# Kernel optimization log

Measured on AMD Instinct MI355X. Metric: run time of the kernel, lower is better.

Reference implementation:

```python
import jax, jax.numpy as jnp
import numpy as np

B, S, DIM = 4, 2048, 2048
H = 16
NOPE, ROPE, VD = 128, 64, 128
QKD = NOPE + ROPE            # 192
KVR = 512                    # kv_lora_rank
SCALE = QKD ** -0.5


def rms_norm(x, w, eps=1e-6):
    return x * jax.lax.rsqrt(jnp.mean(x * x, axis=-1, keepdims=True) + eps) * w


def rotary(x, cos, sin):
    # x: (b, s, h, r) with consecutive (real, imag) pairs; cos/sin: (s, r//2)
    xr, xi = x[..., 0::2], x[..., 1::2]
    c = cos[None, :, None, :]
    s_ = sin[None, :, None, :]
    yr = xr * c - xi * s_
    yi = xr * s_ + xi * c
    # re-interleave pairs -> (..., r)
    return jnp.stack([yr, yi], axis=-1).reshape(x.shape)


def setup_inputs() -> dict:
    key = jax.random.key(0)
    ks = jax.random.split(key, 6)
    w = 0.02
    x = jax.random.normal(ks[0], (B, S, DIM), jnp.float32)
    wq = jax.random.normal(ks[1], (DIM, H * QKD), jnp.float32) * w
    wkv_a = jax.random.normal(ks[2], (DIM, KVR + ROPE), jnp.float32) * w
    kv_norm_w = jnp.ones((KVR,), jnp.float32)
    wkv_b = jax.random.normal(ks[3], (H * (NOPE + VD), KVR), jnp.float32) * w
    wo = jax.random.normal(ks[4], (H * VD, DIM), jnp.float32) * w
    # standard RoPE frequencies for the 64-dim decoupled rope component
    inv_freq = 1.0 / (10000.0 ** (np.arange(0, ROPE, 2, dtype=np.float32) / ROPE))
    t = np.arange(S, dtype=np.float32)
    ang = np.outer(t, inv_freq)  # (S, ROPE//2)
    freqs_cos = jnp.asarray(np.cos(ang), jnp.float32)
    freqs_sin = jnp.asarray(np.sin(ang), jnp.float32)
    # causal mask (start_pos = 0 prefill)
    mask = jnp.where(jnp.triu(jnp.ones((S, S), bool), k=1), jnp.float32(-1e9), jnp.float32(0.0))
    return {"x": x, "wq": wq, "wkv_a": wkv_a, "kv_norm_w": kv_norm_w,
            "wkv_b": wkv_b, "wo": wo, "freqs_cos": freqs_cos,
            "freqs_sin": freqs_sin, "mask": mask}


def reference(x, wq, wkv_a, kv_norm_w, wkv_b, wo, freqs_cos, freqs_sin, mask):
    b, s, _ = x.shape
    # query projection and nope/rope split
    q = (x @ wq).reshape(b, s, H, QKD)
    q_nope, q_pe = q[..., :NOPE], q[..., NOPE:]
    q_pe = rotary(q_pe, freqs_cos, freqs_sin)                 # (b,s,H,ROPE)
    # kv low-rank latent + decoupled rope key
    kv_full = x @ wkv_a                                       # (b,t,KVR+ROPE)
    kv, k_pe = kv_full[..., :KVR], kv_full[..., KVR:]
    k_pe = rotary(k_pe[:, :, None, :], freqs_cos, freqs_sin)[:, :, 0, :]  # (b,t,ROPE)
    # absorb q_nope through wkv_b's key half
    w_b = wkv_b.reshape(H, NOPE + VD, KVR)
    q_abs = jnp.einsum('bshd,hdc->bshc', q_nope, w_b[:, :NOPE])  # (b,s,H,KVR)
    kv_c = rms_norm(kv, kv_norm_w)                            # latent kv cache (b,t,KVR)
    # two-term scores in latent + rope space
    scores = (jnp.einsum('bshc,btc->bsht', q_abs, kv_c)
              + jnp.einsum('bshr,btr->bsht', q_pe, k_pe)) * SCALE
    scores = scores + mask[None, :, None, :]
    attn = jax.nn.softmax(scores.astype(jnp.float32), axis=-1).astype(x.dtype)
    # attend in latent space, then expand with wkv_b's value half
    o = jnp.einsum('bsht,btc->bshc', attn, kv_c)
    o = jnp.einsum('bshc,hdc->bshd', o, w_b[:, NOPE:])        # (b,s,H,VD)
    return o.reshape(b, s, H * VD) @ wo
```

## Files before the change

kernel.cpp:

```cpp
#include <hip/hip_runtime.h>
#include <hip/hip_bf16.h>
#include <cstdio>
#include <cstdint>

#define BB   4
#define SS   2048
#define DIMM 2048
#define HH   16
#define NOPED 128
#define QKD  192
#define KVR  512
#define DQK  576
#define SCALE_F 0.07216878364870323f

typedef __attribute__((ext_vector_type(4))) float f32x4;
typedef __attribute__((ext_vector_type(8))) __bf16 bf16x8;
typedef __attribute__((ext_vector_type(8))) unsigned short u16x8;

__device__ __forceinline__ f32x4 mfma16(bf16x8 a, bf16x8 b, f32x4 c) {
  return __builtin_amdgcn_mfma_f32_16x16x32_bf16(a, b, c, 0, 0, 0);
}

__device__ __forceinline__ void gl16(const __bf16* g, __bf16* l) {
  __builtin_amdgcn_global_load_lds(
      (const __attribute__((address_space(1))) unsigned int*)g,
      (__attribute__((address_space(3))) unsigned int*)l, 16, 0, 0);
}

__global__ void k_cvt(const float* __restrict__ in, __bf16* __restrict__ out, int n) {
  int i = (blockIdx.x * 256 + threadIdx.x) * 8;
  if (i >= n) return;
  float4 a = *(const float4*)(in + i);
  float4 b = *(const float4*)(in + i + 4);
  bf16x8 v;
  v[0] = (__bf16)a.x; v[1] = (__bf16)a.y; v[2] = (__bf16)a.z; v[3] = (__bf16)a.w;
  v[4] = (__bf16)b.x; v[5] = (__bf16)b.y; v[6] = (__bf16)b.z; v[7] = (__bf16)b.w;
  *(bf16x8*)(out + i) = v;
}

__global__ void k_tr(const float* __restrict__ in, __bf16* __restrict__ out,
                     int R, int C, int64_t inBS, int64_t outBS) {
  in  += (int64_t)blockIdx.z * inBS;
  out += (int64_t)blockIdx.z * outBS;
  __shared__ float t[32][33];
  int c0 = blockIdx.x * 32, r0 = blockIdx.y * 32;
#pragma unroll
  for (int i = 0; i < 4; i++) {
    int r = r0 + threadIdx.y + i * 8, c = c0 + threadIdx.x;
    if (r < R && c < C) t[threadIdx.y + i * 8][threadIdx.x] = in[(int64_t)r * C + c];
  }
  __syncthreads();
#pragma unroll
  for (int i = 0; i < 4; i++) {
    int c = c0 + threadIdx.y + i * 8, r = r0 + threadIdx.x;
    if (c < C && r < R) out[(int64_t)c * R + r] = (__bf16)t[threadIdx.x][threadIdx.y + i * 8];
  }
}

template <bool OUTF32>
__global__ __launch_bounds__(256) void k_gemm(
    const __bf16* __restrict__ A, const __bf16* __restrict__ Bt, void* __restrict__ Cv,
    int N, int K, int lda, int ldb, int ldc,
    int64_t aSB, int64_t aSH, int64_t bSH, int64_t cSB, int64_t cSH, int Hdiv, float scale) {
  const int z = blockIdx.z;
  const int zb = z / Hdiv, zh = z % Hdiv;
  const int64_t aBase = zb * aSB + zh * aSH;
  const int64_t bBase = zh * bSH;
  const int64_t cBase = zb * cSB + zh * cSH;
  const int n0 = blockIdx.x * 128, m0 = blockIdx.y * 128;
  const int tid = threadIdx.x, lane = tid & 63, wid = tid >> 6;
  const int p = lane & 15, g = lane >> 4;
  const int wr = (wid >> 1) * 64, wc = (wid & 1) * 64;
  __shared__ alignas(16) __bf16 lA[128 * 32];
  __shared__ alignas(16) __bf16 lB[128 * 32];
  const f32x4 fz = {};
  f32x4 acc[4][4];
#pragma unroll
  for (int i = 0; i < 4; i++)
#pragma unroll
    for (int j = 0; j < 4; j++) acc[i][j] = fz;
  const __bf16* gA0 = A + aBase + (int64_t)(m0 + (tid >> 2)) * lda + (tid & 3) * 8;
  const __bf16* gA1 = A + aBase + (int64_t)(m0 + 64 + (tid >> 2)) * lda + (tid & 3) * 8;
  const __bf16* gB0 = Bt + bBase + (int64_t)(n0 + (tid >> 2)) * ldb + (tid & 3) * 8;
  const __bf16* gB1 = Bt + bBase + (int64_t)(n0 + 64 + (tid >> 2)) * ldb + (tid & 3) * 8;
  auto stage = [&](int kt) {
    gl16(gA0 + kt, &lA[tid * 8]);
    gl16(gA1 + kt, &lA[(256 + tid) * 8]);
    gl16(gB0 + kt, &lB[tid * 8]);
    gl16(gB1 + kt, &lB[(256 + tid) * 8]);
  };
  stage(0);
  for (int kt = 0; kt < K; kt += 32) {
    asm volatile("s_waitcnt vmcnt(0)" ::: "memory");
    __builtin_amdgcn_s_barrier();
    bf16x8 af[4], bfr[4];
#pragma unroll
    for (int mi = 0; mi < 4; mi++) af[mi]  = *(const bf16x8*)&lA[(wr + mi * 16 + p) * 32 + g * 8];
#pragma unroll
    for (int ni = 0; ni < 4; ni++) bfr[ni] = *(const bf16x8*)&lB[(wc + ni * 16 + p) * 32 + g * 8];
#pragma unroll
    for (int mi = 0; mi < 4; mi++)
#pragma unroll
      for (int ni = 0; ni < 4; ni++) acc[mi][ni] = mfma16(af[mi], bfr[ni], acc[mi][ni]);
    asm volatile("s_waitcnt lgkmcnt(0)" ::: "memory");
    __builtin_amdgcn_s_barrier();
    if (kt + 32 < K) stage(kt + 32);
  }
#pragma unroll
  for (int mi = 0; mi < 4; mi++) {
#pragma unroll
    for (int ni = 0; ni < 4; ni++) {
      const int n = n0 + wc + ni * 16 + p;
      if (n < N) {
#pragma unroll
        for (int r = 0; r < 4; r++) {
          const int m = m0 + wr + mi * 16 + g * 4 + r;
          float v = acc[mi][ni][r] * scale;
          if (OUTF32) ((float*)Cv)[cBase + (int64_t)m * ldc + n] = v;
          else        ((__bf16*)Cv)[cBase + (int64_t)m * ldc + n] = (__bf16)v;
        }
      }
    }
  }
}

__global__ __launch_bounds__(64) void k_kvprep(
    const __bf16* __restrict__ kvfull, const float* __restrict__ wnorm,
    const float* __restrict__ fc, const float* __restrict__ fs,
    __bf16* __restrict__ Kcat) {
  const int row = blockIdx.x;
  const int lane = threadIdx.x;
  const int s = row & 2047;
  const __bf16* src = kvfull + (int64_t)row * DQK;
  bf16x8 v = *(const bf16x8*)(src + lane * 8);
  float f[8], ss = 0.f;
#pragma unroll
  for (int j = 0; j < 8; j++) { f[j] = (float)v[j]; ss += f[j] * f[j]; }
#pragma unroll
  for (int mk = 1; mk < 64; mk <<= 1) ss += __shfl_xor(ss, mk, 64);
  float rn = rsqrtf(ss * (1.f / 512.f) + 1e-6f);
  bf16x8 o;
#pragma unroll
  for (int j = 0; j < 8; j++) o[j] = (__bf16)(f[j] * rn * wnorm[lane * 8 + j]);
  *(bf16x8*)(Kcat + (int64_t)row * DQK + lane * 8) = o;
  if (lane < 32) {
    float xr = (float)src[512 + 2 * lane];
    float xi = (float)src[512 + 2 * lane + 1];
    float c = fc[s * 32 + lane], sn = fs[s * 32 + lane];
    Kcat[(int64_t)row * DQK + 512 + 2 * lane]     = (__bf16)(xr * c - xi * sn);
    Kcat[(int64_t)row * DQK + 512 + 2 * lane + 1] = (__bf16)(xr * sn + xi * c);
  }
}

__global__ void k_qpe(const __bf16* __restrict__ qfull, const float* __restrict__ fc,
                      const float* __restrict__ fs, __bf16* __restrict__ Qcat) {
  int idx = blockIdx.x * 256 + threadIdx.x;
  if (idx >= BB * HH * SS * 32) return;
  int i = idx & 31, s = (idx >> 5) & 2047, h = (idx >> 16) & 15, b = idx >> 20;
  const __bf16* src = qfull + ((int64_t)(b * SS + s)) * 3072 + h * QKD + NOPED;
  float xr = (float)src[2 * i], xi = (float)src[2 * i + 1];
  float c = fc[s * 32 + i], sn = fs[s * 32 + i];
  __bf16* dst = Qcat + (((int64_t)(b * HH + h)) * SS + s) * DQK + 512;
  dst[2 * i]     = (__bf16)((xr * c - xi * sn) * SCALE_F);
  dst[2 * i + 1] = (__bf16)((xr * sn + xi * c) * SCALE_F);
}

__global__ __launch_bounds__(256, 2) void k_attn(
    const __bf16* __restrict__ Qcat, const __bf16* __restrict__ Kcat,
    const __bf16* __restrict__ Vt2, __bf16* __restrict__ Ohead) {
  const int gx = blockIdx.x;
  const int w  = blockIdx.y;
  const int z  = gx * 8 + (w & 7);
  const int yv = w >> 3;
  const int kk = yv >> 2, cc = yv & 3;
  const int bx = (kk & 1) ? (31 - ((kk - 1) << 1) - cc) : ((kk << 1) + cc);
  const int b = z >> 4, h = z & 15;
  const int q0 = bx * 64;
  const int tid = threadIdx.x, lane = tid & 63, wid = tid >> 6;
  const int p = lane & 15, g = lane >> 4;
  const int qw = q0 + wid * 16;
  __shared__ alignas(16) __bf16 lK[32 * 576];
  __shared__ alignas(16) __bf16 lV[128 * 32];
  __shared__ alignas(16) __bf16 lP[4 * 512];

  bf16x8 qreg[18];
  {
    const __bf16* qb = Qcat + ((int64_t)z * SS + qw + p) * DQK + g * 8;
#pragma unroll
    for (int kc = 0; kc < 18; kc++) qreg[kc] = *(const bf16x8*)(qb + kc * 32);
  }
  bf16x8 ones;
#pragma unroll
  for (int j = 0; j < 8; j++) ones[j] = (__bf16)1.0f;
  const f32x4 fz = {};
  f32x4 acc[8];
#pragma unroll
  for (int ct = 0; ct < 8; ct++) acc[ct] = fz;
  float mrun[4] = {-1e30f, -1e30f, -1e30f, -1e30f};
  float lrun[4] = {0.f, 0.f, 0.f, 0.f};

  const __bf16* kBase = Kcat + (int64_t)b * SS * DQK;
  const __bf16* vBase = Vt2 + (int64_t)z * 128 * SS;

  auto stage = [&](int t0) {
    const __bf16* kb = kBase + (int64_t)t0 * DQK;
#pragma unroll
    for (int it = 0; it < 9; it++) {
      int slot = it * 256 + tid;
      int row = slot / 72, u = slot - row * 72;
      gl16(kb + row * DQK + ((u ^ (row & 7)) * 8), &lK[(it * 256 + tid) * 8]);
    }
    const __bf16* vb = vBase + t0;
#pragma unroll
    for (int it = 0; it < 2; it++) {
      int slot = it * 256 + tid;
      int c = slot >> 2, u = slot & 3;
      gl16(vb + c * SS + ((u ^ ((c >> 1) & 3)) * 8), &lV[(it * 256 + tid) * 8]);
    }
  };

  const int nsteps = bx * 2 + 2;
  stage(0);
  const int vkey = (p >> 1) & 3;
  for (int st = 0; st < nsteps; st++) {
    const int t0 = st * 32;
    asm volatile("s_waitcnt vmcnt(0)" ::: "memory");
    __builtin_amdgcn_s_barrier();

    __builtin_amdgcn_s_setprio(1);
    f32x4 sca[2], scb[2];
    sca[0] = fz; sca[1] = fz; scb[0] = fz; scb[1] = fz;
#pragma unroll
    for (int kc = 0; kc < 18; kc += 2) {
#pragma unroll
      for (int n = 0; n < 2; n++) {
        int trow = n * 16 + p;
        bf16x8 bf0 = *(const bf16x8*)&lK[trow * 576 + (((4 * kc + g) ^ (trow & 7))) * 8];
        bf16x8 bf1 = *(const bf16x8*)&lK[trow * 576 + (((4 * (kc + 1) + g) ^ (trow & 7))) * 8];
        sca[n] = mfma16(qreg[kc], bf0, sca[n]);
        scb[n] = mfma16(qreg[kc + 1], bf1, scb[n]);
      }
    }
    __builtin_amdgcn_s_setprio(0);
    f32x4 sc[2];
#pragma unroll
    for (int n = 0; n < 2; n++)
#pragma unroll
      for (int r = 0; r < 4; r++) sc[n][r] = sca[n][r] + scb[n][r];
    if (t0 + 31 > qw) {
#pragma unroll
      for (int n = 0; n < 2; n++) {
        int t = t0 + n * 16 + p;
#pragma unroll
        for (int r = 0; r < 4; r++) {
          int q = qw + g * 4 + r;
          if (t > q) sc[n][r] = -1e9f;
        }
      }
    }

    float es[4];
    int needAny = 0;
#pragma unroll
    for (int r = 0; r < 4; r++) {
      float mx = fmaxf(sc[0][r], sc[1][r]);
#pragma unroll
      for (int mk = 1; mk < 16; mk <<= 1) mx = fmaxf(mx, __shfl_xor(mx, mk, 64));
      if (mx > mrun[r] + 8.f) { es[r] = __expf(mrun[r] - mx); mrun[r] = mx; needAny = 1; }
      else es[r] = 1.f;
      float s0 = __expf(sc[0][r] - mrun[r]);
      float s1 = __expf(sc[1][r] - mrun[r]);
      int prow = g * 4 + r;
      int swz = ((prow >> 1) & 3) * 8;
      lP[wid * 512 + prow * 32 + (p ^ swz)]        = (__bf16)s0;
      lP[wid * 512 + prow * 32 + ((16 + p) ^ swz)] = (__bf16)s1;
    }
    if (__any(needAny)) {
#pragma unroll
      for (int ct = 0; ct < 8; ct++)
#pragma unroll
        for (int r = 0; r < 4; r++) acc[ct][r] *= es[r];
    }
    bf16x8 pa = *(const bf16x8*)&lP[wid * 512 + p * 32 + ((g ^ vkey) * 8)];
    {
      f32x4 rs = mfma16(pa, ones, fz);
#pragma unroll
      for (int r = 0; r < 4; r++) lrun[r] = lrun[r] * es[r] + rs[r];
    }

    __builtin_amdgcn_s_setprio(1);
#pragma unroll
    for (int ct = 0; ct < 8; ct++) {
      int c = ct * 16 + p;
      bf16x8 bv = *(const bf16x8*)&lV[c * 32 + ((g ^ vkey) * 8)];
      acc[ct] = mfma16(pa, bv, acc[ct]);
    }
    __builtin_amdgcn_s_setprio(0);
    asm volatile("s_waitcnt lgkmcnt(0)" ::: "memory");
    __builtin_amdgcn_s_barrier();
    if (st + 1 < nsteps) stage(t0 + 32);
  }

#pragma unroll
  for (int r = 0; r < 4; r++) {
    float inv = 1.f / lrun[r];
    int64_t rb = ((int64_t)b * SS + qw + g * 4 + r) * 2048 + h * 128;
#pragma unroll
    for (int ct = 0; ct < 8; ct++) Ohead[rb + ct * 16 + p] = (__bf16)(acc[ct][r] * inv);
  }
}

extern "C" void kernel_launch(void* const* d_in, const int* in_sizes, int n_in,
                              void* d_out, int out_size, void* d_ws, size_t ws_size,
                              hipStream_t stream) {
  const float* x     = (const float*)d_in[0];
  const float* wq    = (const float*)d_in[1];
  const float* wkv_a = (const float*)d_in[2];
  const float* kvw   = (const float*)d_in[3];
  const float* wkv_b = (const float*)d_in[4];
  const float* wo    = (const float*)d_in[5];
  const float* fc    = (const float*)d_in[6];
  const float* fs    = (const float*)d_in[7];
  float* out = (float*)d_out;

  char* base = (char*)d_ws;
  const size_t OFF_KCAT  = 0;
  const size_t OFF_VT    = OFF_KCAT + 9437184ull;
  const size_t OFF_WKVB  = OFF_VT + 8388608ull;
  const size_t OFF_WOT   = OFF_WKVB + 4194304ull;
  const size_t OFF_QCAT  = OFF_WOT + 8388608ull;
  const size_t OFF_OHEAD = OFF_QCAT + 150994944ull;
  const size_t OFF_QFULL = OFF_OHEAD + 33554432ull;
  const size_t TOTAL     = OFF_QFULL + 50331648ull;

  __bf16* Kcat    = (__bf16*)(base + OFF_KCAT);
  __bf16* wkvb_bf = (__bf16*)(base + OFF_WKVB);
  __bf16* woT     = (__bf16*)(base + OFF_WOT);
  __bf16* Qcat    = (__bf16*)(base + OFF_QCAT);
  __bf16* o_head  = (__bf16*)(base + OFF_OHEAD);
  __bf16* qfull   = (__bf16*)(base + OFF_QFULL);
  __bf16* Vt2     = (__bf16*)(base + OFF_QFULL);
  __bf16* wqT    = (__bf16*)(base + OFF_KCAT);
  __bf16* wkvaT  = (__bf16*)(base + OFF_KCAT + 12582912);
  __bf16* xb     = (__bf16*)(base + OFF_QCAT);
  __bf16* kvfull = (__bf16*)(base + OFF_QCAT + 33554432);
  __bf16* wbTn   = (__bf16*)(base + OFF_OHEAD);

  if (ws_size < TOTAL) {
    fprintf(stderr, "kernel_launch: ws too small: need %zu have %zu\n", TOTAL, ws_size);
    return;
  }

  k_cvt<<<8192, 256, 0, stream>>>(x, xb, BB * SS * DIMM);
  k_cvt<<<1024, 256, 0, stream>>>(wkv_b, wkvb_bf, 4096 * 512);
  k_tr<<<dim3(96, 64, 1), dim3(32, 8), 0, stream>>>(wq, wqT, 2048, 3072, 0, 0);
  k_tr<<<dim3(18, 64, 1), dim3(32, 8), 0, stream>>>(wkv_a, wkvaT, 2048, 576, 0, 0);
  k_tr<<<dim3(64, 64, 1), dim3(32, 8), 0, stream>>>(wo, woT, 2048, 2048, 0, 0);
  k_tr<<<dim3(16, 4, 16), dim3(32, 8), 0, stream>>>(wkv_b, wbTn, 128, 512,
                                                    (int64_t)256 * 512, (int64_t)512 * 128);
  k_gemm<false><<<dim3(24, 64, 1), 256, 0, stream>>>(
      xb, wqT, qfull, 3072, 2048, 2048, 2048, 3072, 0, 0, 0, 0, 0, 1, 1.0f);
  k_gemm<false><<<dim3(5, 64, 1), 256, 0, stream>>>(
      xb, wkvaT, kvfull, 576, 2048, 2048, 2048, 576, 0, 0, 0, 0, 0, 1, 1.0f);
  k_kvprep<<<8192, 64, 0, stream>>>(kvfull, kvw, fc, fs, Kcat);
  k_gemm<false><<<dim3(4, 16, 64), 256, 0, stream>>>(
      qfull, wbTn, Qcat, 512, 128, 3072, 128, 576,
      (int64_t)SS * 3072, (int64_t)QKD, (int64_t)512 * 128,
      (int64_t)HH * SS * DQK, (int64_t)SS * DQK, 16, SCALE_F);
  k_qpe<<<16384, 256, 0, stream>>>(qfull, fc, fs, Qcat);
  k_gemm<false><<<dim3(16, 1, 64), 256, 0, stream>>>(
      wkvb_bf + 128 * 512, Kcat, Vt2, 2048, 512, 512, DQK, 2048,
      (int64_t)256 * 512, 0, (int64_t)SS * DQK,
      (int64_t)128 * 2048, (int64_t)16 * 128 * 2048, 4, 1.0f);
  k_attn<<<dim3(8, 256), 256, 0, stream>>>(Qcat, Kcat, Vt2, o_head);
  k_gemm<true><<<dim3(16, 64, 1), 256, 0, stream>>>(
      o_head, woT, out, 2048, 2048, 2048, 2048, 2048, 0, 0, 0, 0, 0, 1, 1.0f);
}
```

Baseline: 772.4 us.

## Use 256x256-tile 512-thread GEMM for Q and output projections

Adds a new GEMM kernel with 256x256 output tiles, 8 waves per block, double-buffered LDS staging through global_load_lds with XOR swizzle, and raised wave priority around the MFMA loop. The Q projection and the final output projection now use it instead of the generic 128x128-style kernel. Larger tiles raise arithmetic intensity and cut global/L2 traffic per FLOP. In exchange they use 128KB of LDS per block and a large accumulator footprint, so occupancy drops, and the grid shrinks to 384 and 256 blocks on a 256-CU part, which risks wave-quantization tail effects.

```diff
diff --git a/kernel.cpp b/kernel.cpp
--- a/kernel.cpp
+++ b/kernel.cpp
@@ -124,6 +124,85 @@
   }
 }
 
+template <bool OUTF32>
+__global__ __launch_bounds__(512) void k_gemm2(
+    const __bf16* __restrict__ A, const __bf16* __restrict__ Bt, void* __restrict__ Cv,
+    int K, int lda, int ldb, int ldc, float scale) {
+  const int n0 = blockIdx.x * 256, m0 = blockIdx.y * 256;
+  const int tid = threadIdx.x, lane = tid & 63, wid = tid >> 6;
+  const int p = lane & 15, g = lane >> 4;
+  const int wm = wid >> 2, wn = wid & 3;
+  __shared__ alignas(16) __bf16 lA[2][256 * 64];
+  __shared__ alignas(16) __bf16 lB[2][256 * 64];
+  const f32x4 fz = {};
+  f32x4 acc[8][4];
+#pragma unroll
+  for (int m = 0; m < 8; m++)
+#pragma unroll
+    for (int n = 0; n < 4; n++) acc[m][n] = fz;
+
+  const int sr = tid >> 3, sg = tid & 7;
+  const int scol = ((sg ^ (sr & 7)) * 8);
+  const __bf16* gA = A + (int64_t)(m0 + sr) * lda + scol;
+  const __bf16* gB = Bt + (int64_t)(n0 + sr) * ldb + scol;
+  auto stage = [&](int t, int buf) {
+    const __bf16* a = gA + t * 64;
+    const __bf16* b = gB + t * 64;
+#pragma unroll
+    for (int it = 0; it < 4; it++) {
+      gl16(a + (int64_t)(it * 64) * lda, &lA[buf][(it * 512 + tid) * 8]);
+      gl16(b + (int64_t)(it * 64) * ldb, &lB[buf][(it * 512 + tid) * 8]);
+    }
+  };
+
+  const int nt = K >> 6;
+  stage(0, 0);
+  for (int t = 0; t < nt; t++) {
+    const int cu = t & 1;
+    asm volatile("s_waitcnt vmcnt(0)" ::: "memory");
+    __builtin_amdgcn_s_barrier();
+    if (t + 1 < nt) stage(t + 1, cu ^ 1);
+
+    bf16x8 bfr[4][2];
+#pragma unroll
+    for (int n = 0; n < 4; n++) {
+      int rb = wn * 64 + n * 16 + p;
+#pragma unroll
+      for (int kk = 0; kk < 2; kk++)
+        bfr[n][kk] = *(const bf16x8*)&lB[cu][rb * 64 + (((kk * 4 + g) ^ (rb & 7)) * 8)];
+    }
+    __builtin_amdgcn_s_setprio(1);
+#pragma unroll
+    for (int m = 0; m < 8; m++) {
+      int ra = wm * 128 + m * 16 + p;
+      bf16x8 a0 = *(const bf16x8*)&lA[cu][ra * 64 + (((0 + g) ^ (ra & 7)) * 8)];
+      bf16x8 a1 = *(const bf16x8*)&lA[cu][ra * 64 + (((4 + g) ^ (ra & 7)) * 8)];
+#pragma unroll
+      for (int n = 0; n < 4; n++) {
+        acc[m][n] = mfma16(a0, bfr[n][0], acc[m][n]);
+        acc[m][n] = mfma16(a1, bfr[n][1], acc[m][n]);
+      }
+    }
+    __builtin_amdgcn_s_setprio(0);
+    asm volatile("s_waitcnt lgkmcnt(0)" ::: "memory");
+  }
+
+#pragma unroll
+  for (int m = 0; m < 8; m++) {
+#pragma unroll
+    for (int n = 0; n < 4; n++) {
+      const int nn = n0 + wn * 64 + n * 16 + p;
+#pragma unroll
+      for (int r = 0; r < 4; r++) {
+        const int mm = m0 + wm * 128 + m * 16 + g * 4 + r;
+        float v = acc[m][n][r] * scale;
+        if (OUTF32) ((float*)Cv)[(int64_t)mm * ldc + nn] = v;
+        else        ((__bf16*)Cv)[(int64_t)mm * ldc + nn] = (__bf16)v;
+      }
+    }
+  }
+}
+
 __global__ __launch_bounds__(64) void k_kvprep(
     const __bf16* __restrict__ kvfull, const float* __restrict__ wnorm,
     const float* __restrict__ fc, const float* __restrict__ fs,
@@ -358,8 +437,8 @@
   k_tr<<<dim3(64, 64, 1), dim3(32, 8), 0, stream>>>(wo, woT, 2048, 2048, 0, 0);
   k_tr<<<dim3(16, 4, 16), dim3(32, 8), 0, stream>>>(wkv_b, wbTn, 128, 512,
                                                     (int64_t)256 * 512, (int64_t)512 * 128);
-  k_gemm<false><<<dim3(24, 64, 1), 256, 0, stream>>>(
-      xb, wqT, qfull, 3072, 2048, 2048, 2048, 3072, 0, 0, 0, 0, 0, 1, 1.0f);
+  k_gemm2<false><<<dim3(12, 32), 512, 0, stream>>>(
+      xb, wqT, qfull, 2048, 2048, 2048, 3072, 1.0f);
   k_gemm<false><<<dim3(5, 64, 1), 256, 0, stream>>>(
       xb, wkvaT, kvfull, 576, 2048, 2048, 2048, 576, 0, 0, 0, 0, 0, 1, 1.0f);
   k_kvprep<<<8192, 64, 0, stream>>>(kvfull, kvw, fc, fs, Kcat);
@@ -373,6 +452,6 @@
       (int64_t)256 * 512, 0, (int64_t)SS * DQK,
       (int64_t)128 * 2048, (int64_t)16 * 128 * 2048, 4, 1.0f);
   k_attn<<<dim3(8, 256), 256, 0, stream>>>(Qcat, Kcat, Vt2, o_head);
-  k_gemm<true><<<dim3(16, 64, 1), 256, 0, stream>>>(
-      o_head, woT, out, 2048, 2048, 2048, 2048, 2048, 0, 0, 0, 0, 0, 1, 1.0f);
-}
+  k_gemm2<true><<<dim3(8, 32), 512, 0, stream>>>(
+      o_head, woT, out, 2048, 2048, 2048, 2048, 1.0f);
+}
```

Result: faster. 747.4 us (-3.2%).
